# Kernel optimization log

Hardware: AMD Instinct MI355X
Metric: run time of the kernel (lower is better)

The kernel has to match this reference:

```python
import jax, jax.numpy as jnp
import numpy as np

# static config (matches init_kwargs / source constants)
B, S, CCH, NF, T = 64, 50, 3, 129, 29   # batch, seq, channels, freq bins (nfft/2+1), frames
M_FB = 32                                # filterbank size M in F1
D = 16                                   # latents -> SPD matrix size
M_OFF = D * (D - 1) // 2                 # strictly-lower Cholesky entries
HID = D + M_OFF                          # ODE state size
ODE_U = 256                              # n_units
NCLS = 5
K_EULER, DT = 4, 0.25                    # fixed-step Euler ODE solve per interval
BN_EPS = 1e-5


def lin_tri_filter(nfilt=M_FB, nfft=256, samplerate=100):
    # faithful port of FilterbankShape.lin_tri_filter_shape
    highfreq = samplerate / 2
    hz = np.linspace(0, highfreq, nfilt + 2)
    b = np.floor((nfft + 1) * hz / samplerate)
    fb = np.zeros([nfilt, nfft // 2 + 1])
    for j in range(nfilt):
        for i in range(int(b[j]), int(b[j + 1])):
            fb[j, i] = (i - b[j]) / (b[j + 1] - b[j])
        for i in range(int(b[j + 1]), int(b[j + 2])):
            fb[j, i] = (b[j + 2] - i) / (b[j + 2] - b[j + 1])
    return fb.T.astype(np.float32)  # (129, 32)


def setup_inputs() -> dict:
    key = jax.random.key(0)
    ks = jax.random.split(key, 32)
    f32 = jnp.float32
    CIN = CCH * M_FB  # 96

    def unif(k, shape, bound):
        return jax.random.uniform(k, shape, f32, -bound, bound)

    sd = 1.0 / np.sqrt(D)
    so = 1.0 / np.sqrt(M_OFF)
    cb1 = 1.0 / np.sqrt(CIN * 5)
    cb2 = 1.0 / np.sqrt(CIN * 5)
    lb = lambda fan_in: 1.0 / np.sqrt(fan_in)

    inp = {
        "x": jax.random.normal(ks[0], (B, S, CCH, NF, T), f32),
        "fw": jax.nn.sigmoid(jax.random.normal(ks[1], (NF, M_FB), f32)),
        "s_tri": jnp.asarray(lin_tri_filter()),
        "conv1_w": unif(ks[2], (CIN, CIN, 5), cb1),
        "conv1_b": unif(ks[3], (CIN,), cb1),
        "bn1_g": jnp.ones((CIN,), f32),
        "bn1_b": jnp.zeros((CIN,), f32),
        "conv2_w": unif(ks[4], (D, CIN, 5), cb2),
        "conv2_b": unif(ks[5], (D,), cb2),
        "bn2_g": jnp.ones((D,), f32),
        "bn2_b": jnp.zeros((D,), f32),
        "wx_d": unif(ks[6], (D, 3 * D), sd),
        "wh_d": unif(ks[7], (D, 3 * D), sd),
        "bias_d": unif(ks[8], (3 * D,), sd),
        "wx_o": unif(ks[9], (M_OFF, 3 * M_OFF), so),
        "wh_o": unif(ks[10], (M_OFF, 3 * M_OFF), so),
        "bias_o": unif(ks[11], (3 * M_OFF,), so),
        "ode_w0": unif(ks[12], (HID, ODE_U), lb(HID)),
        "ode_b0": unif(ks[13], (ODE_U,), lb(HID)),
        "ode_w1": unif(ks[14], (ODE_U, ODE_U), lb(ODE_U)),
        "ode_b1": unif(ks[15], (ODE_U,), lb(ODE_U)),
        "ode_w2": unif(ks[16], (ODE_U, ODE_U), lb(ODE_U)),
        "ode_b2": unif(ks[17], (ODE_U,), lb(ODE_U)),
        "ode_w3": unif(ks[18], (ODE_U, HID), lb(ODE_U)),
        "ode_b3": unif(ks[19], (HID,), lb(ODE_U)),
        "cls_w": unif(ks[20], (HID, NCLS), lb(HID)),
        "cls_b": unif(ks[21], (NCLS,), lb(HID)),
    }
    return inp


def _forward(x, fw, s_tri, conv1_w, conv1_b, bn1_g, bn1_b, conv2_w, conv2_b,
             bn2_g, bn2_b, wx_d, wh_d, bias_d, wx_o, wh_o, bias_o,
             ode_w0, ode_b0, ode_w1, ode_b1, ode_w2, ode_b2, ode_w3, ode_b3,
             cls_w, cls_b):
    b, s = x.shape[:2]
    # --- filter_bank: (b,s,C,F,T) x (F,M) -> (b,s,C*M,T) ---
    xf = jnp.einsum('bscft,fm->bscmt', x, fw * s_tri)
    h = xf.reshape(b * s, CCH * M_FB, T)
    dn = ('NCH', 'OIH', 'NCH')

    def conv_bn_lrelu(h, w, bias, g, be):
        h = jax.lax.conv_general_dilated(h, w, (1,), 'VALID', dimension_numbers=dn)
        h = h + bias[None, :, None]
        mu = h.mean((0, 2), keepdims=True)           # BatchNorm1d (train-mode stats)
        var = h.var((0, 2), keepdims=True)
        h = (h - mu) / jnp.sqrt(var + BN_EPS) * g[None, :, None] + be[None, :, None]
        return jnp.where(h >= 0, h, 0.01 * h)        # LeakyReLU

    h = conv_bn_lrelu(h, conv1_w, conv1_b, bn1_g, bn1_b)   # (bs, 96, 25)
    h = conv_bn_lrelu(h, conv2_w, conv2_b, bn2_g, bn2_b)   # (bs, D, 21)
    feats = h.transpose(0, 2, 1)                           # (bs, t, D)

    def oas(X):  # OAS-shrunk covariance, X: (n, d)
        n, d = X.shape
        xm = X - X.mean(0)
        emp = xm.T @ xm / (n - 1)
        mu = jnp.trace(emp) / d
        alpha = jnp.mean(emp ** 2)
        num = alpha + mu ** 2
        den = (n + 1.0) * (alpha - mu ** 2 / d)
        shr = jnp.where(den == 0, 1.0, jnp.minimum(num / den, 1.0))
        return (1.0 - shr) * emp + shr * mu * jnp.eye(d, dtype=X.dtype)

    covs = jax.vmap(oas)(feats)                            # (bs, D, D)
    L = jnp.linalg.cholesky(covs).reshape(b, s, D, D)
    ir, ic = np.tril_indices(D, -1)
    x_d = jnp.diagonal(L, axis1=-2, axis2=-1)              # (b,s,D) positive
    x_o = L[..., ir, ic]                                   # (b,s,M_OFF)

    def ode_net(hh):  # odefunc: Lin, [Tanh,Lin]*2, Tanh, Lin
        hh = hh @ ode_w0 + ode_b0
        hh = jnp.tanh(hh) @ ode_w1 + ode_b1
        hh = jnp.tanh(hh) @ ode_w2 + ode_b2
        return jnp.tanh(hh) @ ode_w3 + ode_b3

    abs_bd = jnp.abs(bias_d)

    def step(carry, xt):
        hd, ho = carry
        xd, xo = xt
        # ODE evolution of hidden state in Cholesky chart (log-diag || off-diag)
        hc = jnp.concatenate([jnp.log(hd), ho], -1)
        for _ in range(K_EULER):
            hc = hc + DT * ode_net(hc)
        hd = jnp.exp(hc[:, :D])
        ho = hc[:, D:]
        # diag RGRU cell (PosLinear + softplus; log/exp products simplify)
        gx = xd @ jnp.abs(wx_d)
        gh = hd @ jnp.abs(wh_d)
        ixr, ixi, ixn = jnp.split(gx, 3, 1)
        hhr, hhi, hhn = jnp.split(gh, 3, 1)
        br, bi, bn = jnp.split(abs_bd, 3)
        r = jax.nn.sigmoid(br * ixr * hhr)
        z = jax.nn.sigmoid(bi * ixi * hhi)
        ng = jax.nn.softplus(bn * ixn * r * hhn)
        hd = hd ** z * ng ** (1.0 - z)   # geodesic GRU update on positive diag
        # off-diag RGRU cell (standard Euclidean GRU)
        gx = xo @ wx_o
        gh = ho @ wh_o
        ixr, ixi, ixn = jnp.split(gx, 3, 1)
        hhr, hhi, hhn = jnp.split(gh, 3, 1)
        br2, bi2, bn2 = jnp.split(bias_o, 3)
        r = jax.nn.sigmoid(ixr + hhr + br2)
        z = jax.nn.sigmoid(ixi + hhi + bi2)
        ng = jnp.tanh(ixn + r * hhn + bn2)
        ho = ng + z * (ho - ng)
        return (hd, ho), None

    hd0 = jnp.ones((b, D), x.dtype)
    ho0 = jnp.zeros((b, M_OFF), x.dtype)
    (hd, ho), _ = jax.lax.scan(step, (hd0, ho0),
                               (x_d.transpose(1, 0, 2), x_o.transpose(1, 0, 2)))
    feat = jnp.concatenate([jnp.log(hd), ho], -1)
    return feat @ cls_w + cls_b  # (b, NCLS)


def reference(x, fw, s_tri, conv1_w, conv1_b, bn1_g, bn1_b, conv2_w, conv2_b,
              bn2_g, bn2_b, wx_d, wh_d, bias_d, wx_o, wh_o, bias_o,
              ode_w0, ode_b0, ode_w1, ode_b1, ode_w2, ode_b2, ode_w3, ode_b3,
              cls_w, cls_b):
    return _forward(x, fw, s_tri, conv1_w, conv1_b, bn1_g, bn1_b, conv2_w,
                    conv2_b, bn2_g, bn2_b, wx_d, wh_d, bias_d, wx_o, wh_o,
                    bias_o, ode_w0, ode_b0, ode_w1, ode_b1, ode_w2, ode_b2,
                    ode_w3, ode_b3, cls_w, cls_b)
```

## Files before the change

kernel.cpp:

```cpp
#include <hip/hip_runtime.h>
#include <math.h>


#define BB 64
#define NIMG 3200

typedef _Float16 f16;
typedef _Float16 f16x8 __attribute__((ext_vector_type(8)));
typedef float f32x4 __attribute__((ext_vector_type(4)));

#define HS 164
#define GS 516

__device__ __forceinline__ float fsigm(float x) {
  return __fdividef(1.f, 1.f + __expf(-x));
}
__device__ __forceinline__ float ftanh(float x) {
  return 1.f - __fdividef(2.f, __expf(2.f * x) + 1.f);
}

#define OFF_W0  0
#define OFF_W1  20480
#define OFF_W2  53248
#define OFF_W3  86016
#define OFF_GRZ 104448
#define OFF_GNX 135168
#define OFF_GNH 143360
#define PK2_TOT 151552

__global__ __launch_bounds__(256) void k0b_w1h(const float* __restrict__ w,
                                               f16* __restrict__ dst) {
  int i = blockIdx.x * 256 + threadIdx.x;
  if (i < 46080) dst[i] = (f16)w[i];
}

__global__ __launch_bounds__(256) void k1_fb(const float* __restrict__ x,
                                             const float* __restrict__ fw,
                                             const float* __restrict__ st,
                                             float* __restrict__ h1) {
  __shared__ __align__(16) float ws[129 * 32];
  __shared__ __align__(16) float xs[129 * 32];
  const int tid = threadIdx.x;
  const int n = blockIdx.x;
  const float* xp = x + (size_t)n * 11223;

  for (int i = tid; i < 4128; i += 256) ws[i] = fw[i] * st[i];

  float acc[4][4];
#pragma unroll
  for (int i = 0; i < 4; ++i)
#pragma unroll
    for (int j = 0; j < 4; ++j) acc[i][j] = 0.f;

  const int c = tid / 64;
  const int rem = tid % 64;
  const int m0 = (rem / 8) * 4;
  const int t0 = (rem % 8) * 4;

  for (int fc = 0; fc < 3; ++fc) {
    __syncthreads();
    for (int i = tid; i < 3741; i += 256) {
      int cc = i / 1247;
      int r = i - cc * 1247;
      int f = r / 29;
      int t = r - f * 29;
      xs[(cc * 43 + f) * 32 + t] = xp[cc * 3741 + (fc * 43 + f) * 29 + t];
    }
    for (int i = tid; i < 129; i += 256) {
      xs[i * 32 + 29] = 0.f; xs[i * 32 + 30] = 0.f; xs[i * 32 + 31] = 0.f;
    }
    __syncthreads();
    if (tid < 192) {
      const float* xb = xs + (c * 43) * 32 + t0;
      const float* wb = ws + (fc * 43) * 32 + m0;
      for (int f = 0; f < 43; ++f) {
        float4 xv = *(const float4*)(xb + f * 32);
        float4 wv = *(const float4*)(wb + f * 32);
        float xa[4] = {xv.x, xv.y, xv.z, xv.w};
        float wa[4] = {wv.x, wv.y, wv.z, wv.w};
#pragma unroll
        for (int i = 0; i < 4; ++i)
#pragma unroll
          for (int j = 0; j < 4; ++j) acc[i][j] += wa[i] * xa[j];
      }
    }
  }
  if (tid < 192) {
    const int nt = (t0 == 28) ? 1 : 4;
    for (int i = 0; i < 4; ++i)
      for (int j = 0; j < nt; ++j)
        h1[(size_t)n * 2784 + (size_t)(c * 32 + m0 + i) * 29 + (t0 + j)] = acc[i][j];
  }
}

__global__ __launch_bounds__(256) void k2_conv1(const float* __restrict__ h1,
                                                const f16* __restrict__ wh,
                                                const float* __restrict__ bias,
                                                float* __restrict__ h2,
                                                float* __restrict__ part1) {
  __shared__ __align__(16) float ins[2 * 96 * 32];
  __shared__ __align__(16) f16 wls[96 * 81 + 8];
  const int tid = threadIdx.x;
  const int wg = blockIdx.x;

  for (int i = tid; i < 2 * 2784; i += 256) {
    int img = i / 2784;
    int e = i - img * 2784;
    int ci = e / 29;
    int t = e - ci * 29;
    ins[img * 3072 + ci * 32 + t] = h1[(size_t)(wg * 2 + img) * 2784 + e];
  }

  const int img = tid / 96;
  const int co = tid - img * 96;
  float acc[25];
#pragma unroll
  for (int t = 0; t < 25; ++t) acc[t] = 0.f;

  for (int cc = 0; cc < 6; ++cc) {
    __syncthreads();
    for (int i = tid; i < 7680; i += 256) {
      int cw = i / 80;
      int r = i - cw * 80;
      wls[cw * 81 + r] = wh[cw * 480 + cc * 80 + r];
    }
    __syncthreads();
    if (tid < 192) {
      for (int ci = 0; ci < 16; ++ci) {
        float xv[32];
        const float4* xr = (const float4*)&ins[img * 3072 + (cc * 16 + ci) * 32];
#pragma unroll
        for (int q = 0; q < 8; ++q) *(float4*)&xv[4 * q] = xr[q];
        float wv[5];
#pragma unroll
        for (int d = 0; d < 5; ++d) wv[d] = (float)wls[co * 81 + ci * 5 + d];
#pragma unroll
        for (int t = 0; t < 25; ++t) {
          float s = acc[t];
#pragma unroll
          for (int d = 0; d < 5; ++d) s += xv[t + d] * wv[d];
          acc[t] = s;
        }
      }
    }
  }
  if (tid < 192) {
    const int n = wg * 2 + img;
    const float bval = bias[co];
    float s1 = 0.f, s2 = 0.f;
    for (int t = 0; t < 25; ++t) {
      float v = acc[t] + bval;
      h2[(size_t)n * 2400 + co * 25 + t] = v;
      s1 += v;
      s2 += v * v;
    }
    part1[((size_t)n * 96 + co) * 2 + 0] = s1;
    part1[((size_t)n * 96 + co) * 2 + 1] = s2;
  }
}

__global__ __launch_bounds__(256) void k3_bn1(const float* __restrict__ part,
                                              const float* __restrict__ gg,
                                              const float* __restrict__ be,
                                              float* __restrict__ ab) {
  __shared__ double sd[256], sq[256];
  const int c = blockIdx.x;
  const int t = threadIdx.x;
  double s = 0.0, q = 0.0;
  for (int n = t; n < NIMG; n += 256) {
    s += (double)part[((size_t)n * 96 + c) * 2 + 0];
    q += (double)part[((size_t)n * 96 + c) * 2 + 1];
  }
  sd[t] = s; sq[t] = q;
  __syncthreads();
  for (int off = 128; off > 0; off >>= 1) {
    if (t < off) { sd[t] += sd[t + off]; sq[t] += sq[t + off]; }
    __syncthreads();
  }
  if (t == 0) {
    double mu = sd[0] / 80000.0;
    double var = sq[0] / 80000.0 - mu * mu;
    float A = (float)((double)gg[c] / sqrt(var + 1e-5));
    ab[c * 2 + 0] = A;
    ab[c * 2 + 1] = (float)((double)be[c] - mu * (double)A);
  }
}

__global__ __launch_bounds__(256) void k5_bn2(const float* __restrict__ part,
                                              const float* __restrict__ gg,
                                              const float* __restrict__ be,
                                              float* __restrict__ ab) {
  __shared__ double sd[256], sq[256];
  const int c = blockIdx.x;
  const int t = threadIdx.x;
  double s = 0.0, q = 0.0;
  for (int n = t; n < 800; n += 256) {
    s += (double)part[((size_t)n * 16 + c) * 2 + 0];
    q += (double)part[((size_t)n * 16 + c) * 2 + 1];
  }
  sd[t] = s; sq[t] = q;
  __syncthreads();
  for (int off = 128; off > 0; off >>= 1) {
    if (t < off) { sd[t] += sd[t + off]; sq[t] += sq[t + off]; }
    __syncthreads();
  }
  if (t == 0) {
    double mu = sd[0] / 67200.0;
    double var = sq[0] / 67200.0 - mu * mu;
    float A = (float)((double)gg[c] / sqrt(var + 1e-5));
    ab[c * 2 + 0] = A;
    ab[c * 2 + 1] = (float)((double)be[c] - mu * (double)A);
  }
}

__global__ __launch_bounds__(256) void k4_conv2(const float* __restrict__ h2,
                                                const float* __restrict__ w,
                                                const float* __restrict__ bias,
                                                const float* __restrict__ bn1,
                                                float* __restrict__ h3,
                                                float* __restrict__ part2) {
  __shared__ __align__(16) float ins[4 * 96 * 26];
  __shared__ __align__(16) float wls[16 * 241];
  __shared__ float A1s[96], B1s[96];
  __shared__ float red[16 * 16 * 2];
  const int tid = threadIdx.x;
  const int wg = blockIdx.x;

  if (tid < 96) {
    A1s[tid] = bn1[tid * 2 + 0];
    B1s[tid] = bn1[tid * 2 + 1];
  }
  __syncthreads();
  for (int i = tid; i < 9600; i += 256) {
    int img = i / 2400;
    int e = i - img * 2400;
    int ci = e / 25;
    int t = e - ci * 25;
    float v = h2[(size_t)(wg * 4 + img) * 2400 + e];
    v = A1s[ci] * v + B1s[ci];
    v = (v >= 0.f) ? v : 0.01f * v;
    ins[img * 2496 + ci * 26 + t] = v;
  }
  for (int i = tid; i < 4 * 96; i += 256) ins[(i / 96) * 2496 + (i % 96) * 26 + 25] = 0.f;

  const int img = tid >> 6;
  const int co = (tid >> 2) & 15;
  const int tg = tid & 3;
  const int t0s[4] = {0, 6, 11, 16};
  const int t0 = t0s[tg];
  const int tl = (tg == 0) ? 6 : 5;
  float acc[6] = {0.f, 0.f, 0.f, 0.f, 0.f, 0.f};

  for (int cc = 0; cc < 2; ++cc) {
    __syncthreads();
    for (int i = tid; i < 3840; i += 256) {
      int cw = i / 240;
      int r = i - cw * 240;
      wls[cw * 241 + r] = w[cw * 480 + cc * 240 + r];
    }
    __syncthreads();
    for (int ci = 0; ci < 48; ++ci) {
      float xv[10];
#pragma unroll
      for (int j = 0; j < 10; ++j) xv[j] = ins[img * 2496 + (cc * 48 + ci) * 26 + t0 + j];
      float wv[5];
#pragma unroll
      for (int d = 0; d < 5; ++d) wv[d] = wls[co * 241 + ci * 5 + d];
#pragma unroll
      for (int t = 0; t < 6; ++t) {
        float s = acc[t];
#pragma unroll
        for (int d = 0; d < 5; ++d) s += xv[t + d] * wv[d];
        acc[t] = s;
      }
    }
  }
  const float bval = bias[co];
  float s1 = 0.f, s2 = 0.f;
  const int n = wg * 4 + img;
  for (int t = 0; t < 6; ++t) {
    if (t < tl) {
      float v = acc[t] + bval;
      h3[(size_t)n * 336 + co * 21 + t0 + t] = v;
      s1 += v;
      s2 += v * v;
    }
  }
  red[(co * 16 + img * 4 + tg) * 2 + 0] = s1;
  red[(co * 16 + img * 4 + tg) * 2 + 1] = s2;
  __syncthreads();
  if (tid < 16) {
    float s = 0.f, q = 0.f;
    for (int k = 0; k < 16; ++k) {
      s += red[(tid * 16 + k) * 2 + 0];
      q += red[(tid * 16 + k) * 2 + 1];
    }
    part2[((size_t)wg * 16 + tid) * 2 + 0] = s;
    part2[((size_t)wg * 16 + tid) * 2 + 1] = q;
  }
}

__global__ __launch_bounds__(256) void k6_oas(const float* __restrict__ h3,
                                              const float* __restrict__ bn2,
                                              float* __restrict__ xd,
                                              float* __restrict__ xo) {
  __shared__ float X[4][21 * 17 + 3];
  __shared__ float A[4][16 * 17];
  __shared__ float mcol[4][16];
  const int tid = threadIdx.x;
  const int wid = tid >> 6;
  const int lane = tid & 63;
  const int n = blockIdx.x * 4 + wid;
  const float* hp = h3 + (size_t)n * 336;

  for (int e = lane; e < 336; e += 64) {
    int c = e / 21;
    int t = e - c * 21;
    float v = hp[e];
    v = bn2[c * 2 + 0] * v + bn2[c * 2 + 1];
    v = (v >= 0.f) ? v : 0.01f * v;
    X[wid][t * 17 + c] = v;
  }
  __syncthreads();
  if (lane < 16) {
    float s = 0.f;
    for (int t = 0; t < 21; ++t) s += X[wid][t * 17 + lane];
    mcol[wid][lane] = s * (1.f / 21.f);
  }
  __syncthreads();
  for (int e = lane; e < 336; e += 64) {
    int t = e / 16;
    int c = e - t * 16;
    X[wid][t * 17 + c] -= mcol[wid][c];
  }
  __syncthreads();

  float tr_p = 0.f, al_p = 0.f;
  float ent[3];
  int ei[3], ej[3], ne = 0;
  for (int e = lane; e < 136; e += 64) {
    int i = 0, e2 = e;
    while (e2 >= 16 - i) { e2 -= 16 - i; i++; }
    int j = i + e2;
    float s = 0.f;
    for (int t = 0; t < 21; ++t) s += X[wid][t * 17 + i] * X[wid][t * 17 + j];
    s *= (1.f / 20.f);
    ent[ne] = s; ei[ne] = i; ej[ne] = j; ne++;
    if (i == j) tr_p += s;
    al_p += s * s * ((i == j) ? 1.f : 2.f);
  }
  for (int m = 1; m < 64; m <<= 1) {
    tr_p += __shfl_xor(tr_p, m);
    al_p += __shfl_xor(al_p, m);
  }
  const float mu = tr_p * (1.f / 16.f);
  const float alpha = al_p * (1.f / 256.f);
  const float num = alpha + mu * mu;
  const float den = 22.f * (alpha - mu * mu * (1.f / 16.f));
  const float shr = (den == 0.f) ? 1.f : fminf(num / den, 1.f);
  for (int q = 0; q < ne; ++q) {
    float c = (1.f - shr) * ent[q] + ((ei[q] == ej[q]) ? shr * mu : 0.f);
    A[wid][ei[q] * 17 + ej[q]] = c;
    A[wid][ej[q] * 17 + ei[q]] = c;
  }
  __syncthreads();

  for (int k = 0; k < 16; ++k) {
    float akk = A[wid][k * 17 + k];
    __syncthreads();
    float d = sqrtf(akk);
    float rd = 1.f / d;
    if (lane == k) A[wid][k * 17 + k] = d;
    if (lane > k && lane < 16) A[wid][lane * 17 + k] *= rd;
    __syncthreads();
    if (lane > k && lane < 16) {
      float Lik = A[wid][lane * 17 + k];
      for (int j = k + 1; j <= lane; ++j) A[wid][lane * 17 + j] -= Lik * A[wid][j * 17 + k];
    }
    __syncthreads();
  }
  if (lane < 16) xd[(size_t)n * 16 + lane] = A[wid][lane * 17 + lane];
  for (int p = lane; p < 120; p += 64) {
    int i = 1, p2 = p;
    while (p2 >= i) { p2 -= i; i++; }
    xo[(size_t)n * 120 + p] = A[wid][i * 17 + p2];
  }
}

__global__ __launch_bounds__(256) void k0_pack(const float* __restrict__ w0,
                                               const float* __restrict__ w1,
                                               const float* __restrict__ w2,
                                               const float* __restrict__ w3,
                                               const float* __restrict__ wxo,
                                               const float* __restrict__ who,
                                               uint32_t* __restrict__ dst) {
  int i = blockIdx.x * 256 + threadIdx.x;
  if (i >= PK2_TOT) return;
  int j = i, kind, NT;
  if (j < OFF_W1)       { kind = 0; NT = 16; }
  else if (j < OFF_W2)  { kind = 1; NT = 16; j -= OFF_W1; }
  else if (j < OFF_W3)  { kind = 2; NT = 16; j -= OFF_W2; }
  else if (j < OFF_GRZ) { kind = 3; NT = 9;  j -= OFF_W3; }
  else if (j < OFF_GNX) { kind = 4; NT = 15; j -= OFF_GRZ; }
  else if (j < OFF_GNH) { kind = 5; NT = 8;  j -= OFF_GNX; }
  else                  { kind = 6; NT = 8;  j -= OFF_GNH; }
  const int tile = j >> 8;
  const int rem = j & 255;
  const int l = rem >> 2;
  const int wd = rem & 3;
  const int t = tile / NT;
  const int nt = tile - t * NT;
  const int col = nt * 16 + (l & 15);
  const int kk = t * 32 + 8 * (l >> 4) + 2 * wd;

  float v[2];
#pragma unroll
  for (int q = 0; q < 2; ++q) {
    const int k = kk + q;
    float s = 0.f;
    if (kind == 0)      { if (k < 136) s = w0[k * 256 + col]; }
    else if (kind == 1) { s = w1[k * 256 + col]; }
    else if (kind == 2) { s = w2[k * 256 + col]; }
    else if (kind == 3) { if (col < 136) s = w3[k * 136 + col]; }
    else if (kind == 4) {
      if (k < 120) s = wxo[k * 360 + col];
      else if (k >= 128 && k < 248) s = who[(k - 128) * 360 + col];
    } else if (kind == 5) { if (k < 120 && col < 120) s = wxo[k * 360 + 240 + col]; }
    else                  { if (k < 120 && col < 120) s = who[k * 360 + 240 + col]; }
    v[q] = s;
  }
  union { f16 h[2]; uint32_t u; } cv;
  cv.h[0] = (f16)v[0];
  cv.h[1] = (f16)v[1];
  dst[i] = cv.u;
}

__device__ __forceinline__ uint4 aread_lin(const f16* X, int t, int l) {
  return ((const uint4*)X)[t * 64 + l];
}
__device__ __forceinline__ void xwrite_frag(f16* X, int row, int col, float v) {
  const int slot = row + 16 * ((col >> 3) & 3);
  const int byte = (((col >> 5) * 64 + slot) << 4) + 2 * (col & 7);
  *(f16*)((char*)X + byte) = (f16)v;
}

union UF { uint4 u; f16x8 h; };

template <int KT, int NT>
__device__ __forceinline__ void mlp_pf(const f16* __restrict__ Xin,
                                       const float* __restrict__ bias,
                                       f16* __restrict__ Xout,
                                       int nt, int l,
                                       uint4 (&bf)[8],
                                       const uint4* __restrict__ B2,
                                       int NT2, int nt2, int nkt2) {
  const int m = l & 15;
  const int g = l >> 4;
  const bool act = (nt >= 0 && nt < NT);
  f32x4 acc = {0.f, 0.f, 0.f, 0.f};
#pragma unroll
  for (int t = 0; t < 8; ++t) {
    if (t < KT && act) {
      UF a; a.u = aread_lin(Xin, t, l);
      UF b; b.u = bf[t];
      acc = __builtin_amdgcn_mfma_f32_16x16x32_f16(a.h, b.h, acc, 0, 0, 0);
    }
    if (nt2 >= 0 && t < nkt2) bf[t] = B2[(t * NT2 + nt2) * 64 + l];
  }
  if (!act) return;
  const int col = nt * 16 + m;
  const float bb = bias[col];
#pragma unroll
  for (int i2 = 0; i2 < 4; ++i2)
    xwrite_frag(Xout, 4 * g + i2, col, ftanh(acc[i2] + bb));
}

template <int MODE>
__device__ __forceinline__ void mlp_lds(const f16* __restrict__ Xin,
                                        const uint4* __restrict__ W3s,
                                        const float* __restrict__ bias,
                                        float* __restrict__ hcf,
                                        f16* __restrict__ Xnext,
                                        float* __restrict__ ehl,
                                        int nt, int l) {
  if (nt < 0) return;
  const int m = l & 15;
  const int g = l >> 4;
  f32x4 acc = {0.f, 0.f, 0.f, 0.f};
#pragma unroll
  for (int t = 0; t < 8; ++t) {
    UF a; a.u = aread_lin(Xin, t, l);
    UF b; b.u = W3s[(t * 9 + nt) * 64 + l];
    acc = __builtin_amdgcn_mfma_f32_16x16x32_f16(a.h, b.h, acc, 0, 0, 0);
  }
  const int col = nt * 16 + m;
  if (col < 136) {
    const float bb = bias[col];
#pragma unroll
    for (int i2 = 0; i2 < 4; ++i2) {
      const int row = 4 * g + i2;
      float v = hcf[row * HS + col] + 0.25f * (acc[i2] + bb);
      hcf[row * HS + col] = v;
      if (MODE == 1) {
        xwrite_frag(Xnext, row, col, v);
      } else {
        if (col >= 16) xwrite_frag(Xnext, row, col + 112, v);
        else ehl[row * 16 + col] = __expf(v);
      }
    }
  }
}

template <int KT, int NT>
__device__ __forceinline__ void gate_rz(const f16* __restrict__ Xin,
                                        float* __restrict__ GO,
                                        int nt, int gooff, int l,
                                        uint4 (&bf)[8]) {
  if (nt < 0) return;
  const int m = l & 15;
  const int g = l >> 4;
  f32x4 acc = {0.f, 0.f, 0.f, 0.f};
#pragma unroll
  for (int t = 0; t < KT; ++t) {
    UF a; a.u = aread_lin(Xin, t, l);
    UF b; b.u = bf[t];
    acc = __builtin_amdgcn_mfma_f32_16x16x32_f16(a.h, b.h, acc, 0, 0, 0);
  }
  const int col = nt * 16 + m;
#pragma unroll
  for (int i2 = 0; i2 < 4; ++i2)
    GO[(4 * g + i2) * GS + gooff + col] = acc[i2];
}

template <int KT, int NT>
__device__ __forceinline__ void gate_tile(const f16* __restrict__ Xin,
                                          const uint4* __restrict__ B,
                                          float* __restrict__ GO,
                                          int nt, int ktoff, int gooff, int l) {
  if (nt < 0) return;
  const int m = l & 15;
  const int g = l >> 4;
  uint4 bfx[KT];
#pragma unroll
  for (int t = 0; t < KT; ++t) bfx[t] = B[(t * NT + nt) * 64 + l];
  f32x4 acc = {0.f, 0.f, 0.f, 0.f};
#pragma unroll
  for (int t = 0; t < KT; ++t) {
    UF a; a.u = aread_lin(Xin, t + ktoff, l);
    UF b; b.u = bfx[t];
    acc = __builtin_amdgcn_mfma_f32_16x16x32_f16(a.h, b.h, acc, 0, 0, 0);
  }
  const int col = nt * 16 + m;
#pragma unroll
  for (int i2 = 0; i2 < 4; ++i2)
    GO[(4 * g + i2) * GS + gooff + col] = acc[i2];
}

__global__ __launch_bounds__(1024, 1) void k7_scan(
    const float* __restrict__ xdv, const float* __restrict__ xov,
    const float* __restrict__ wxd, const float* __restrict__ whd,
    const float* __restrict__ bdv, const float* __restrict__ bov,
    const uint32_t* __restrict__ pk,
    const float* __restrict__ b0, const float* __restrict__ b1,
    const float* __restrict__ b2, const float* __restrict__ b3,
    const float* __restrict__ cw, const float* __restrict__ cbv,
    float* __restrict__ out) {
  __shared__ __align__(16) f16 XA[16 * 256];
  __shared__ __align__(16) f16 XB[16 * 256];
  __shared__ __align__(16) f16 XG[16 * 256];
  __shared__ __align__(16) uint4 W3s[4608];
  __shared__ __align__(16) float GO[16 * GS];
  __shared__ __align__(16) float hcf[16 * HS];
  __shared__ __align__(16) float xdlv[16 * 16];
  __shared__ __align__(16) float ehl[16 * 16];
  __shared__ __align__(16) float G2[16 * 96];
  __shared__ __align__(16) float wdaT[48 * 16], whaT[48 * 16];
  __shared__ float b0l[256], b1l[256], b2l[256], b3l[144], bovl[360], bdvl[48];

  const int tid = threadIdx.x;
  const int w = tid >> 6;
  const int l = tid & 63;
  const int blk = blockIdx.x;

  const uint4* BW0 = (const uint4*)(pk + OFF_W0);
  const uint4* BW1 = (const uint4*)(pk + OFF_W1);
  const uint4* BW2 = (const uint4*)(pk + OFF_W2);
  const uint4* BW3 = (const uint4*)(pk + OFF_W3);
  const uint4* BRZ = (const uint4*)(pk + OFF_GRZ);
  const uint4* BNX = (const uint4*)(pk + OFF_GNX);
  const uint4* BNH = (const uint4*)(pk + OFF_GNH);

  for (int i = tid; i < 4608; i += 1024) W3s[i] = BW3[i];
  for (int i = tid; i < 768; i += 1024) {
    int k = i / 48, c = i - k * 48;
    wdaT[c * 16 + k] = fabsf(wxd[i]);
    whaT[c * 16 + k] = fabsf(whd[i]);
  }
  for (int i = tid; i < 256; i += 1024) { b0l[i] = b0[i]; b1l[i] = b1[i]; b2l[i] = b2[i]; }
  if (tid < 144) b3l[tid] = (tid < 136) ? b3[tid] : 0.f;
  if (tid < 360) bovl[tid] = bov[tid];
  if (tid < 48) bdvl[tid] = fabsf(bdv[tid]);
  for (int i = tid; i < 16 * HS; i += 1024) hcf[i] = 0.f;
  for (int i = tid; i < 4096; i += 1024) { XA[i] = (f16)0.f; XG[i] = (f16)0.f; }

  uint4 bf[8];
#pragma unroll
  for (int t = 0; t < 5; ++t) bf[t] = BW0[(t * 16 + w) * 64 + l];
  __syncthreads();

#pragma unroll 1
  for (int s = 0; s < 50; ++s) {
#pragma unroll 1
    for (int e = 0; e < 4; ++e) {
      mlp_pf<5, 16>(XA, b0l, XB, w, l, bf, BW1, 16, w, 8);
      if (e == 0) {
        for (int i = tid; i < 1920; i += 1024) {
          int row = i / 120, c = i - row * 120;
          xwrite_frag(XG, row, c, xov[((size_t)(blk * 16 + row) * 50 + s) * 120 + c]);
        }
        if (tid < 256) {
          int row = tid >> 4, k = tid & 15;
          xdlv[tid] = xdv[((size_t)(blk * 16 + row) * 50 + s) * 16 + k];
        }
      }
      __syncthreads();
      mlp_pf<8, 16>(XB, b1l, XA, w, l, bf, BW2, 16, w, 8);
      __syncthreads();
      {
        const uint4* nb = (e == 3) ? BRZ : BW0;
        const int nNT = (e == 3) ? 15 : 16;
        const int nnt = (e == 3) ? ((w < 15) ? w : -1) : w;
        const int nk = (e == 3) ? 8 : 5;
        mlp_pf<8, 16>(XA, b2l, XB, w, l, bf, nb, nNT, nnt, nk);
      }
      __syncthreads();
      if (e < 3)
        mlp_lds<1>(XB, W3s, b3l, hcf, XA, nullptr, (w < 9) ? w : -1, l);
      else
        mlp_lds<2>(XB, W3s, b3l, hcf, XG, ehl, (w < 9) ? w : -1, l);
      __syncthreads();
    }

    gate_rz<8, 15>(XG, GO, (w < 15) ? w : -1, 0, l, bf);
    gate_tile<4, 8>(XG, BNX, GO, (w < 8) ? w : -1, 0, 256, l);
    gate_tile<4, 8>(XG, BNH, GO, (w >= 8) ? (w - 8) : -1, 4, 384, l);
    for (int i = tid; i < 1536; i += 1024) {
      int row = i / 96, c = i - row * 96;
      const float4* sv = (const float4*)((c < 48) ? &xdlv[row * 16] : &ehl[row * 16]);
      const float4* wv = (const float4*)((c < 48) ? &wdaT[c * 16] : &whaT[(c - 48) * 16]);
      float a = 0.f;
#pragma unroll
      for (int q = 0; q < 4; ++q) {
        float4 xq = sv[q], wq = wv[q];
        a += xq.x * wq.x + xq.y * wq.y + xq.z * wq.z + xq.w * wq.w;
      }
      G2[row * 96 + c] = a;
    }
    __syncthreads();

#pragma unroll
    for (int t = 0; t < 5; ++t) bf[t] = BW0[(t * 16 + w) * 64 + l];
    for (int i = tid; i < 1920; i += 1024) {
      int row = i / 120, e2 = i - row * 120;
      float rr = fsigm(GO[row * GS + e2] + bovl[e2]);
      float zz = fsigm(GO[row * GS + 120 + e2] + bovl[120 + e2]);
      float ng = ftanh(GO[row * GS + 256 + e2] + rr * GO[row * GS + 384 + e2] + bovl[240 + e2]);
      float ho = hcf[row * HS + 16 + e2];
      float v = ng + zz * (ho - ng);
      hcf[row * HS + 16 + e2] = v;
      xwrite_frag(XA, row, 16 + e2, v);
    }
    if (tid < 256) {
      int row = tid >> 4, t = tid & 15;
      float ixr = G2[row * 96 + t], ixi = G2[row * 96 + 16 + t], ixn = G2[row * 96 + 32 + t];
      float hhr = G2[row * 96 + 48 + t], hhi = G2[row * 96 + 64 + t], hhn = G2[row * 96 + 80 + t];
      float br = bdvl[t], bi = bdvl[16 + t], bn = bdvl[32 + t];
      float rr = fsigm(br * ixr * hhr);
      float zz = fsigm(bi * ixi * hhi);
      float sp = bn * ixn * rr * hhn;
      float ng = (sp > 20.f) ? sp : __logf(1.f + __expf(sp));
      float ldp = hcf[row * HS + t];
      float v = zz * ldp + (1.f - zz) * __logf(ng);
      hcf[row * HS + t] = v;
      xwrite_frag(XA, row, t, v);
    }
    __syncthreads();
  }

  if (tid < 80) {
    int row = tid / 5, c = tid - row * 5;
    float a = cbv[c];
    for (int k = 0; k < 136; ++k) a += hcf[row * HS + k] * cw[k * 5 + c];
    out[(size_t)(blk * 16 + row) * 5 + c] = a;
  }
}

extern "C" void kernel_launch(void* const* d_in, const int* in_sizes, int n_in,
                              void* d_out, int out_size, void* d_ws, size_t ws_size,
                              hipStream_t stream) {
  const float* x       = (const float*)d_in[0];
  const float* fw      = (const float*)d_in[1];
  const float* s_tri   = (const float*)d_in[2];
  const float* conv1_w = (const float*)d_in[3];
  const float* conv1_b = (const float*)d_in[4];
  const float* bn1_g   = (const float*)d_in[5];
  const float* bn1_b   = (const float*)d_in[6];
  const float* conv2_w = (const float*)d_in[7];
  const float* conv2_b = (const float*)d_in[8];
  const float* bn2_g   = (const float*)d_in[9];
  const float* bn2_b   = (const float*)d_in[10];
  const float* wx_d    = (const float*)d_in[11];
  const float* wh_d    = (const float*)d_in[12];
  const float* bias_d  = (const float*)d_in[13];
  const float* wx_o    = (const float*)d_in[14];
  const float* wh_o    = (const float*)d_in[15];
  const float* bias_o  = (const float*)d_in[16];
  const float* ode_w0  = (const float*)d_in[17];
  const float* ode_b0  = (const float*)d_in[18];
  const float* ode_w1  = (const float*)d_in[19];
  const float* ode_b1  = (const float*)d_in[20];
  const float* ode_w2  = (const float*)d_in[21];
  const float* ode_b2  = (const float*)d_in[22];
  const float* ode_w3  = (const float*)d_in[23];
  const float* ode_b3  = (const float*)d_in[24];
  const float* cls_w   = (const float*)d_in[25];
  const float* cls_b   = (const float*)d_in[26];

  float* ws = (float*)d_ws;
  float* h1  = ws;
  float* h3  = ws;
  float* xd  = ws + 1075200;
  float* xo  = ws + 1126400;
  float* h2  = ws + 8908800;
  float* p1  = ws + 16588800;
  float* bn1 = ws + 17203200;
  float* p2  = ws + 17203392;
  float* bn2 = ws + 17228992;
  f16*   cw1h = (f16*)(ws + 17229024);
  uint32_t* pk = (uint32_t*)(ws + 8908800);

  hipLaunchKernelGGL(k0b_w1h, dim3(180),    dim3(256), 0, stream, conv1_w, cw1h);
  hipLaunchKernelGGL(k1_fb,   dim3(NIMG),   dim3(256), 0, stream, x, fw, s_tri, h1);
  hipLaunchKernelGGL(k2_conv1,dim3(NIMG/2), dim3(256), 0, stream, h1, cw1h, conv1_b, h2, p1);
  hipLaunchKernelGGL(k3_bn1,  dim3(96),     dim3(256), 0, stream, p1, bn1_g, bn1_b, bn1);
  hipLaunchKernelGGL(k4_conv2,dim3(NIMG/4), dim3(256), 0, stream, h2, conv2_w, conv2_b, bn1, h3, p2);
  hipLaunchKernelGGL(k5_bn2,  dim3(16),     dim3(256), 0, stream, p2, bn2_g, bn2_b, bn2);
  hipLaunchKernelGGL(k6_oas,  dim3(NIMG/4), dim3(256), 0, stream, h3, bn2, xd, xo);
  hipLaunchKernelGGL(k0_pack, dim3((PK2_TOT + 255) / 256), dim3(256), 0, stream,
                     ode_w0, ode_w1, ode_w2, ode_w3, wx_o, wh_o, pk);
  hipLaunchKernelGGL(k7_scan, dim3(4),      dim3(1024), 0, stream,
                     xd, xo, wx_d, wh_d, bias_d, bias_o, pk,
                     ode_b0, ode_b1, ode_b2, ode_b3, cls_w, cls_b, (float*)d_out);
}
```

Baseline: 1.543 ms.

## Fuse filterbank into conv1 kernel and use wave barriers in OAS kernel

Merges the filterbank projection and the first convolution into one kernel. Each block now computes the filterbank output for two images straight into shared memory, so the h1 intermediate no longer takes a global-memory round trip or a separate launch. Separately, the per-image OAS/Cholesky kernel swaps its block-wide __syncthreads for wave barriers, since each wave works only on its own image's shared-memory slices. The fused kernel uses much more LDS per block and runs half as many blocks for the filterbank stage, which may reduce occupancy while the input is being streamed.

```diff
diff --git a/kernel.cpp b/kernel.cpp
--- a/kernel.cpp
+++ b/kernel.cpp
@@ -34,88 +34,73 @@
   if (i < 46080) dst[i] = (f16)w[i];
 }
 
-__global__ __launch_bounds__(256) void k1_fb(const float* __restrict__ x,
-                                             const float* __restrict__ fw,
-                                             const float* __restrict__ st,
-                                             float* __restrict__ h1) {
+__global__ __launch_bounds__(256) void k12_fused(const float* __restrict__ x,
+                                                 const float* __restrict__ fw,
+                                                 const float* __restrict__ st,
+                                                 const f16* __restrict__ wh,
+                                                 const float* __restrict__ bias,
+                                                 float* __restrict__ h2,
+                                                 float* __restrict__ part1) {
   __shared__ __align__(16) float ws[129 * 32];
   __shared__ __align__(16) float xs[129 * 32];
+  __shared__ __align__(16) float ins[2 * 96 * 32];
+  __shared__ __align__(16) f16 wls[96 * 81 + 8];
   const int tid = threadIdx.x;
-  const int n = blockIdx.x;
-  const float* xp = x + (size_t)n * 11223;
+  const int wg = blockIdx.x;
 
   for (int i = tid; i < 4128; i += 256) ws[i] = fw[i] * st[i];
-
-  float acc[4][4];
-#pragma unroll
-  for (int i = 0; i < 4; ++i)
-#pragma unroll
-    for (int j = 0; j < 4; ++j) acc[i][j] = 0.f;
 
   const int c = tid / 64;
   const int rem = tid % 64;
   const int m0 = (rem / 8) * 4;
   const int t0 = (rem % 8) * 4;
 
-  for (int fc = 0; fc < 3; ++fc) {
-    __syncthreads();
-    for (int i = tid; i < 3741; i += 256) {
-      int cc = i / 1247;
-      int r = i - cc * 1247;
-      int f = r / 29;
-      int t = r - f * 29;
-      xs[(cc * 43 + f) * 32 + t] = xp[cc * 3741 + (fc * 43 + f) * 29 + t];
-    }
-    for (int i = tid; i < 129; i += 256) {
-      xs[i * 32 + 29] = 0.f; xs[i * 32 + 30] = 0.f; xs[i * 32 + 31] = 0.f;
-    }
-    __syncthreads();
+  for (int img = 0; img < 2; ++img) {
+    const float* xp = x + (size_t)(wg * 2 + img) * 11223;
+    float acc[4][4];
+#pragma unroll
+    for (int i = 0; i < 4; ++i)
+#pragma unroll
+      for (int j = 0; j < 4; ++j) acc[i][j] = 0.f;
+
+    for (int fc = 0; fc < 3; ++fc) {
+      __syncthreads();
+      for (int i = tid; i < 3741; i += 256) {
+        int cc = i / 1247;
+        int r = i - cc * 1247;
+        int f = r / 29;
+        int t = r - f * 29;
+        xs[(cc * 43 + f) * 32 + t] = xp[cc * 3741 + (fc * 43 + f) * 29 + t];
+      }
+      __syncthreads();
+      if (tid < 192) {
+        const float* xb = xs + (c * 43) * 32 + t0;
+        const float* wb = ws + (fc * 43) * 32 + m0;
+        for (int f = 0; f < 43; ++f) {
+          float4 xv = *(const float4*)(xb + f * 32);
+          float4 wv = *(const float4*)(wb + f * 32);
+          float xa[4] = {xv.x, xv.y, xv.z, xv.w};
+          float wa[4] = {wv.x, wv.y, wv.z, wv.w};
+#pragma unroll
+          for (int i = 0; i < 4; ++i)
+#pragma unroll
+            for (int j = 0; j < 4; ++j) acc[i][j] += wa[i] * xa[j];
+        }
+      }
+    }
     if (tid < 192) {
-      const float* xb = xs + (c * 43) * 32 + t0;
-      const float* wb = ws + (fc * 43) * 32 + m0;
-      for (int f = 0; f < 43; ++f) {
-        float4 xv = *(const float4*)(xb + f * 32);
-        float4 wv = *(const float4*)(wb + f * 32);
-        float xa[4] = {xv.x, xv.y, xv.z, xv.w};
-        float wa[4] = {wv.x, wv.y, wv.z, wv.w};
-#pragma unroll
-        for (int i = 0; i < 4; ++i)
-#pragma unroll
-          for (int j = 0; j < 4; ++j) acc[i][j] += wa[i] * xa[j];
-      }
-    }
-  }
-  if (tid < 192) {
-    const int nt = (t0 == 28) ? 1 : 4;
-    for (int i = 0; i < 4; ++i)
-      for (int j = 0; j < nt; ++j)
-        h1[(size_t)n * 2784 + (size_t)(c * 32 + m0 + i) * 29 + (t0 + j)] = acc[i][j];
-  }
-}
-
-__global__ __launch_bounds__(256) void k2_conv1(const float* __restrict__ h1,
-                                                const f16* __restrict__ wh,
-                                                const float* __restrict__ bias,
-                                                float* __restrict__ h2,
-                                                float* __restrict__ part1) {
-  __shared__ __align__(16) float ins[2 * 96 * 32];
-  __shared__ __align__(16) f16 wls[96 * 81 + 8];
-  const int tid = threadIdx.x;
-  const int wg = blockIdx.x;
-
-  for (int i = tid; i < 2 * 2784; i += 256) {
-    int img = i / 2784;
-    int e = i - img * 2784;
-    int ci = e / 29;
-    int t = e - ci * 29;
-    ins[img * 3072 + ci * 32 + t] = h1[(size_t)(wg * 2 + img) * 2784 + e];
+      const int nt = (t0 == 28) ? 1 : 4;
+      for (int i = 0; i < 4; ++i)
+        for (int j = 0; j < nt; ++j)
+          ins[img * 3072 + (c * 32 + m0 + i) * 32 + (t0 + j)] = acc[i][j];
+    }
   }
 
   const int img = tid / 96;
   const int co = tid - img * 96;
-  float acc[25];
-#pragma unroll
-  for (int t = 0; t < 25; ++t) acc[t] = 0.f;
+  float acc2[25];
+#pragma unroll
+  for (int t = 0; t < 25; ++t) acc2[t] = 0.f;
 
   for (int cc = 0; cc < 6; ++cc) {
     __syncthreads();
@@ -136,10 +121,10 @@
         for (int d = 0; d < 5; ++d) wv[d] = (float)wls[co * 81 + ci * 5 + d];
 #pragma unroll
         for (int t = 0; t < 25; ++t) {
-          float s = acc[t];
+          float s = acc2[t];
 #pragma unroll
           for (int d = 0; d < 5; ++d) s += xv[t + d] * wv[d];
-          acc[t] = s;
+          acc2[t] = s;
         }
       }
     }
@@ -149,7 +134,7 @@
     const float bval = bias[co];
     float s1 = 0.f, s2 = 0.f;
     for (int t = 0; t < 25; ++t) {
-      float v = acc[t] + bval;
+      float v = acc2[t] + bval;
       h2[(size_t)n * 2400 + co * 25 + t] = v;
       s1 += v;
       s2 += v * v;
@@ -300,6 +285,7 @@
   }
 }
 
+#define WB() __builtin_amdgcn_wave_barrier()
 __global__ __launch_bounds__(256) void k6_oas(const float* __restrict__ h3,
                                               const float* __restrict__ bn2,
                                               float* __restrict__ xd,
@@ -321,19 +307,19 @@
     v = (v >= 0.f) ? v : 0.01f * v;
     X[wid][t * 17 + c] = v;
   }
-  __syncthreads();
+  WB();
   if (lane < 16) {
     float s = 0.f;
     for (int t = 0; t < 21; ++t) s += X[wid][t * 17 + lane];
     mcol[wid][lane] = s * (1.f / 21.f);
   }
-  __syncthreads();
+  WB();
   for (int e = lane; e < 336; e += 64) {
     int t = e / 16;
     int c = e - t * 16;
     X[wid][t * 17 + c] -= mcol[wid][c];
   }
-  __syncthreads();
+  WB();
 
   float tr_p = 0.f, al_p = 0.f;
   float ent[3];
@@ -363,21 +349,21 @@
     A[wid][ei[q] * 17 + ej[q]] = c;
     A[wid][ej[q] * 17 + ei[q]] = c;
   }
-  __syncthreads();
+  WB();
 
   for (int k = 0; k < 16; ++k) {
     float akk = A[wid][k * 17 + k];
-    __syncthreads();
+    WB();
     float d = sqrtf(akk);
     float rd = 1.f / d;
     if (lane == k) A[wid][k * 17 + k] = d;
     if (lane > k && lane < 16) A[wid][lane * 17 + k] *= rd;
-    __syncthreads();
+    WB();
     if (lane > k && lane < 16) {
       float Lik = A[wid][lane * 17 + k];
       for (int j = k + 1; j <= lane; ++j) A[wid][lane * 17 + j] -= Lik * A[wid][j * 17 + k];
     }
-    __syncthreads();
+    WB();
   }
   if (lane < 16) xd[(size_t)n * 16 + lane] = A[wid][lane * 17 + lane];
   for (int p = lane; p < 120; p += 64) {
@@ -727,7 +713,6 @@
   const float* cls_b   = (const float*)d_in[26];
 
   float* ws = (float*)d_ws;
-  float* h1  = ws;
   float* h3  = ws;
   float* xd  = ws + 1075200;
   float* xo  = ws + 1126400;
@@ -739,16 +724,15 @@
   f16*   cw1h = (f16*)(ws + 17229024);
   uint32_t* pk = (uint32_t*)(ws + 8908800);
 
-  hipLaunchKernelGGL(k0b_w1h, dim3(180),    dim3(256), 0, stream, conv1_w, cw1h);
-  hipLaunchKernelGGL(k1_fb,   dim3(NIMG),   dim3(256), 0, stream, x, fw, s_tri, h1);
-  hipLaunchKernelGGL(k2_conv1,dim3(NIMG/2), dim3(256), 0, stream, h1, cw1h, conv1_b, h2, p1);
-  hipLaunchKernelGGL(k3_bn1,  dim3(96),     dim3(256), 0, stream, p1, bn1_g, bn1_b, bn1);
-  hipLaunchKernelGGL(k4_conv2,dim3(NIMG/4), dim3(256), 0, stream, h2, conv2_w, conv2_b, bn1, h3, p2);
-  hipLaunchKernelGGL(k5_bn2,  dim3(16),     dim3(256), 0, stream, p2, bn2_g, bn2_b, bn2);
-  hipLaunchKernelGGL(k6_oas,  dim3(NIMG/4), dim3(256), 0, stream, h3, bn2, xd, xo);
-  hipLaunchKernelGGL(k0_pack, dim3((PK2_TOT + 255) / 256), dim3(256), 0, stream,
+  hipLaunchKernelGGL(k0b_w1h,  dim3(180),    dim3(256), 0, stream, conv1_w, cw1h);
+  hipLaunchKernelGGL(k12_fused,dim3(NIMG/2), dim3(256), 0, stream, x, fw, s_tri, cw1h, conv1_b, h2, p1);
+  hipLaunchKernelGGL(k3_bn1,   dim3(96),     dim3(256), 0, stream, p1, bn1_g, bn1_b, bn1);
+  hipLaunchKernelGGL(k4_conv2, dim3(NIMG/4), dim3(256), 0, stream, h2, conv2_w, conv2_b, bn1, h3, p2);
+  hipLaunchKernelGGL(k5_bn2,   dim3(16),     dim3(256), 0, stream, p2, bn2_g, bn2_b, bn2);
+  hipLaunchKernelGGL(k6_oas,   dim3(NIMG/4), dim3(256), 0, stream, h3, bn2, xd, xo);
+  hipLaunchKernelGGL(k0_pack,  dim3((PK2_TOT + 255) / 256), dim3(256), 0, stream,
                      ode_w0, ode_w1, ode_w2, ode_w3, wx_o, wh_o, pk);
-  hipLaunchKernelGGL(k7_scan, dim3(4),      dim3(1024), 0, stream,
+  hipLaunchKernelGGL(k7_scan,  dim3(4),      dim3(1024), 0, stream,
                      xd, xo, wx_d, wh_d, bias_d, bias_o, pk,
                      ode_b0, ode_b1, ode_b2, ode_b3, cls_w, cls_b, (float*)d_out);
 }
```

After: 1.628 ms. 5.5% more time.
